# Kernel tuning notes

Hardware: AMD Instinct MI355X
Metric: run time of the kernel (lower is better)

The kernel has to match this reference:

```python
import jax, jax.numpy as jnp
import numpy as np

EPS = 1e-6  # torch nn.PairwiseDistance / TripletMarginLoss default eps (added elementwise to the difference)


def setup_inputs() -> dict:
    key = jax.random.key(0)
    k1, k2, k3, k4 = jax.random.split(key, 4)
    bs, d, n_classes = 4096, 2048, 64
    return {
        "h1": jax.random.normal(k1, (bs, d), dtype=jnp.float32),
        "h2": jax.random.normal(k2, (bs, d), dtype=jnp.float32),
        "labels1": jax.random.randint(k3, (bs,), 0, n_classes, dtype=jnp.int64),
        "labels2": jax.random.randint(k4, (bs,), 0, n_classes, dtype=jnp.int64),
    }


def _pairwise_dist_matrix(h1, h2):
    # torch PairwiseDistance: ||x - y + eps||_2. Expand the square to avoid
    # materializing the (bs, bs, d) broadcast tensor the torch code creates:
    d = h1.shape[-1]
    sq1 = jnp.sum(h1 * h1, axis=-1)          # (bs,)
    sq2 = jnp.sum(h2 * h2, axis=-1)          # (bs,)
    s1 = jnp.sum(h1, axis=-1)                # (bs,)
    s2 = jnp.sum(h2, axis=-1)                # (bs,)
    dot = jnp.einsum("id,jd->ij", h1, h2)   # (bs, bs) -- dominant GEMM
    dist2 = (sq1[:, None] + sq2[None, :] - 2.0 * dot
             + 2.0 * EPS * (s1[:, None] - s2[None, :]) + d * EPS * EPS)
    return jnp.sqrt(jnp.maximum(dist2, 0.0))


def reference(h1, h2, labels1, labels2):
    bs = h1.shape[0]
    h1 = h1.reshape(bs, -1)
    h2 = h2.reshape(bs, -1)

    dist_matrix = _pairwise_dist_matrix(h1, h2)              # (bs, bs)
    label_matrix = labels1[:, None] == labels2[None, :]       # (bs, bs) bool
    valid = jnp.any(label_matrix, axis=-1) & jnp.any(~label_matrix, axis=-1)

    # Hard positive: farthest same-label; hard negative: closest different-label.
    hard_pos_ids = jnp.argmax(jnp.where(label_matrix, dist_matrix, -jnp.inf), axis=-1)
    hard_neg_ids = jnp.argmin(jnp.where(label_matrix, jnp.inf, dist_matrix), axis=-1)

    pos = h2[hard_pos_ids]                                    # (bs, d) gather
    neg = h2[hard_neg_ids]                                    # (bs, d) gather

    d_ap = jnp.sqrt(jnp.sum(jnp.square(h1 - pos + EPS), axis=-1))
    d_an = jnp.sqrt(jnp.sum(jnp.square(h1 - neg + EPS), axis=-1))
    per_row = jnp.maximum(d_ap - d_an, 0.0)                   # margin = 0.0

    cnt = jnp.sum(valid.astype(jnp.float32))
    loss_sum = jnp.sum(jnp.where(valid, per_row, 0.0))
    # Matches torch: mean over valid triples, 0.0 if none are valid.
    return jnp.where(cnt > 0, loss_sum / jnp.maximum(cnt, 1.0), 0.0)
```

## Files before the change

kernel.cpp:

```cpp
#include <hip/hip_runtime.h>
#include <hip/hip_bf16.h>
#include <math.h>

#define BS 4096
#define DIM 2048
#define EPSV 1e-6f

typedef unsigned char u8;
typedef unsigned long long u64;
typedef long i64;
typedef float f32x4 __attribute__((ext_vector_type(4)));

__device__ inline u8 f2e4m3(float f) {
  unsigned u = __float_as_uint(f);
  unsigned s = (u >> 24) & 0x80u;
  unsigned ae = u & 0x7FFFFFFFu;
  if (ae < 0x3C800000u) return (u8)s;
  if (ae > 0x43E00000u) ae = 0x43E00000u;
  unsigned r = ae + 0x7FFFFu + ((ae >> 20) & 1u);
  unsigned e = (r >> 23) & 0xFFu;
  return (u8)(s | ((e - 120u) << 3) | ((r >> 20) & 7u));
}

__device__ inline void gload16(const u8* g, u8* l_) {
  __builtin_amdgcn_global_load_lds((const __attribute__((address_space(1))) unsigned int*)g,
                                   (__attribute__((address_space(3))) unsigned int*)l_,
                                   16, 0, 0);
}

__global__ __launch_bounds__(256) void prep_kernel(
    const float* __restrict__ h1, const float* __restrict__ h2,
    u8* __restrict__ A, u8* __restrict__ B,
    float* __restrict__ sq1, float* __restrict__ s1,
    float* __restrict__ sq2, float* __restrict__ s2) {
  int b = blockIdx.x;
  const float* src; u8* dst; float* sqo; float* so; int row;
  if (b < BS) { src = h1; dst = A; sqo = sq1; so = s1; row = b; }
  else        { src = h2; dst = B; sqo = sq2; so = s2; row = b - BS; }
  src += (size_t)row * DIM;
  dst += (size_t)row * DIM;
  int t = threadIdx.x;
  int idx = t * 8;
  float4 v0 = *(const float4*)(src + idx);
  float4 v1 = *(const float4*)(src + idx + 4);
  float sq = v0.x*v0.x + v0.y*v0.y + v0.z*v0.z + v0.w*v0.w
           + v1.x*v1.x + v1.y*v1.y + v1.z*v1.z + v1.w*v1.w;
  float s  = v0.x + v0.y + v0.z + v0.w + v1.x + v1.y + v1.z + v1.w;
  u64 pk = (u64)f2e4m3(v0.x)
         | ((u64)f2e4m3(v0.y) << 8)
         | ((u64)f2e4m3(v0.z) << 16)
         | ((u64)f2e4m3(v0.w) << 24)
         | ((u64)f2e4m3(v1.x) << 32)
         | ((u64)f2e4m3(v1.y) << 40)
         | ((u64)f2e4m3(v1.z) << 48)
         | ((u64)f2e4m3(v1.w) << 56);
  int vswz = (row >> 2) & 3;
  int dstIdx = (t >> 2) * 32 + (((t & 3) ^ vswz) << 3);
  *(u64*)(dst + dstIdx) = pk;
#pragma unroll
  for (int m = 32; m; m >>= 1) { sq += __shfl_xor(sq, m, 64); s += __shfl_xor(s, m, 64); }
  __shared__ float lsq[4], ls[4];
  if ((t & 63) == 0) { lsq[t >> 6] = sq; ls[t >> 6] = s; }
  __syncthreads();
  if (t == 0) {
    sqo[row] = lsq[0] + lsq[1] + lsq[2] + lsq[3];
    so[row]  = ls[0] + ls[1] + ls[2] + ls[3];
  }
}

#define BK 32
#define NT (DIM / BK)

__global__ __launch_bounds__(512, 4) void gemm_select_kernel(
    const u8* __restrict__ A, const u8* __restrict__ B,
    const float* __restrict__ sq1, const float* __restrict__ s1,
    const float* __restrict__ sq2, const float* __restrict__ s2,
    const int* __restrict__ lab1, const int* __restrict__ lab2,
    float4* __restrict__ part) {
  __shared__ __align__(16) u8 lds[2][12288];
  int tid = threadIdx.x;
  int w = tid >> 6, l = tid & 63;
  int wr = w >> 1, wc = w & 1;
  int g = l >> 4, c = l & 15;
  int by = blockIdx.x >> 5, bx = blockIdx.x & 31;
  const int rowB = by * 256, colB = bx * 128;

  int srow = tid >> 1;
  int khalf = (tid & 1) * 16;
  const u8* gA = A + (size_t)(rowB + srow) * DIM + khalf;
  const u8* gB = B + (size_t)(colB + (srow & 127)) * DIM + khalf;

#define STAGE(T) do { int b_ = (T) & 1; size_t k_ = (size_t)(T) * BK;  \
    gload16(gA + k_, &lds[b_][tid * 16]);                               \
    if (tid < 256) gload16(gB + k_, &lds[b_][8192 + tid * 16]); } while (0)

  const int slot = (g ^ ((c >> 2) & 3)) * 8;

  f32x4 acc[4][4] = {};

  STAGE(0);
  __syncthreads();

  for (int kt = 0; kt < NT; ++kt) {
    const u8* buf = lds[kt & 1];
    if (kt + 1 < NT) STAGE(kt + 1);
    i64 af[4], bfr[4];
#pragma unroll
    for (int mi = 0; mi < 4; ++mi)
      af[mi] = *(const i64*)&buf[(wr * 64 + mi * 16 + c) * 32 + slot];
#pragma unroll
    for (int ni = 0; ni < 4; ++ni)
      bfr[ni] = *(const i64*)&buf[8192 + (wc * 64 + ni * 16 + c) * 32 + slot];
#pragma unroll
    for (int mi = 0; mi < 4; ++mi)
#pragma unroll
      for (int ni = 0; ni < 4; ++ni)
        acc[mi][ni] = __builtin_amdgcn_mfma_f32_16x16x32_fp8_fp8(af[mi], bfr[ni], acc[mi][ni], 0, 0, 0);
    __syncthreads();
  }
#undef STAGE

  float pc_[4]; int l2v[4]; int jcol[4];
#pragma unroll
  for (int ni = 0; ni < 4; ++ni) {
    int j = colB + wc * 64 + ni * 16 + c;
    jcol[ni] = j;
    l2v[ni] = lab2[j];
    pc_[ni] = sq2[j] - 2.0f * EPSV * s2[j];
  }
  const float cst = (float)DIM * EPSV * EPSV;
  int partCol = bx * 2 + wc;

#pragma unroll
  for (int mi = 0; mi < 4; ++mi) {
    float posV[4], negV[4]; int posI[4], negI[4];
    float pr[4]; int l1v[4];
#pragma unroll
    for (int r = 0; r < 4; ++r) {
      int i = rowB + wr * 64 + mi * 16 + g * 4 + r;
      l1v[r] = lab1[i];
      pr[r] = sq1[i] + 2.0f * EPSV * s1[i] + cst;
      posV[r] = -3.0e38f; posI[r] = 0x7fffffff;
      negV[r] =  3.0e38f; negI[r] = 0x7fffffff;
    }
#pragma unroll
    for (int ni = 0; ni < 4; ++ni) {
#pragma unroll
      for (int r = 0; r < 4; ++r) {
        float dot = acc[mi][ni][r];
        float d2 = pr[r] + pc_[ni] - 2.0f * dot;
        float dist = sqrtf(fmaxf(d2, 0.0f));
        bool same = (l1v[r] == l2v[ni]);
        float pv = same ? dist : -3.0e38f;
        float nv = same ?  3.0e38f : dist;
        if (pv > posV[r] || (pv == posV[r] && jcol[ni] < posI[r])) { posV[r] = pv; posI[r] = jcol[ni]; }
        if (nv < negV[r] || (nv == negV[r] && jcol[ni] < negI[r])) { negV[r] = nv; negI[r] = jcol[ni]; }
      }
    }
#pragma unroll
    for (int m = 1; m < 16; m <<= 1) {
#pragma unroll
      for (int r = 0; r < 4; ++r) {
        float ov = __shfl_xor(posV[r], m, 64);
        int   oi = __shfl_xor(posI[r], m, 64);
        if (ov > posV[r] || (ov == posV[r] && oi < posI[r])) { posV[r] = ov; posI[r] = oi; }
        float nv2 = __shfl_xor(negV[r], m, 64);
        int   on  = __shfl_xor(negI[r], m, 64);
        if (nv2 < negV[r] || (nv2 == negV[r] && on < negI[r])) { negV[r] = nv2; negI[r] = on; }
      }
    }
    if (c == 0) {
#pragma unroll
      for (int r = 0; r < 4; ++r) {
        int i = rowB + wr * 64 + mi * 16 + g * 4 + r;
        float4 o;
        o.x = posV[r]; o.y = __int_as_float(posI[r]);
        o.z = negV[r]; o.w = __int_as_float(negI[r]);
        part[(size_t)i * 64 + partCol] = o;
      }
    }
  }
}

__global__ __launch_bounds__(256) void reduce_kernel(const float4* __restrict__ part,
                                                     float* __restrict__ perrow,
                                                     float* __restrict__ validf) {
  int row = blockIdx.x * 4 + (threadIdx.x >> 6);
  int lane = threadIdx.x & 63;
  float4 p = part[(size_t)row * 64 + lane];
  float posV = p.x; int posI = __float_as_int(p.y);
  float negV = p.z; int negI = __float_as_int(p.w);
#pragma unroll
  for (int m = 1; m < 64; m <<= 1) {
    float ov = __shfl_xor(posV, m, 64);
    int   oi = __shfl_xor(posI, m, 64);
    if (ov > posV || (ov == posV && oi < posI)) { posV = ov; posI = oi; }
    float nv = __shfl_xor(negV, m, 64);
    int   on = __shfl_xor(negI, m, 64);
    if (nv < negV || (nv == negV && on < negI)) { negV = nv; negI = on; }
  }
  if (lane == 0) {
    bool valid = (posV > -1.0e38f && negV < 1.0e38f);
    perrow[row] = valid ? fmaxf(posV - negV, 0.0f) : 0.0f;
    validf[row] = valid ? 1.0f : 0.0f;
  }
}

__global__ __launch_bounds__(256) void finalize_kernel(const float* __restrict__ perrow,
                                                       const float* __restrict__ validf,
                                                       float* __restrict__ out) {
  int t = threadIdx.x;
  float s = 0.f, cv = 0.f;
  for (int i = t; i < BS; i += 256) { s += perrow[i]; cv += validf[i]; }
  __shared__ float ls[256], lc[256];
  ls[t] = s; lc[t] = cv;
  __syncthreads();
  for (int m = 128; m; m >>= 1) {
    if (t < m) { ls[t] += ls[t + m]; lc[t] += lc[t + m]; }
    __syncthreads();
  }
  if (t == 0) out[0] = (lc[0] > 0.f) ? ls[0] / fmaxf(lc[0], 1.f) : 0.f;
}

extern "C" void kernel_launch(void* const* d_in, const int* in_sizes, int n_in,
                              void* d_out, int out_size, void* d_ws, size_t ws_size,
                              hipStream_t stream) {
  const float* h1 = (const float*)d_in[0];
  const float* h2 = (const float*)d_in[1];
  const int* lab1 = (const int*)d_in[2];
  const int* lab2 = (const int*)d_in[3];

  char* ws = (char*)d_ws;
  u8* A = (u8*)ws;
  u8* B = (u8*)(ws + (size_t)BS * DIM);
  size_t off = (size_t)BS * DIM * 2;
  float* sq1 = (float*)(ws + off); off += BS * 4;
  float* s1  = (float*)(ws + off); off += BS * 4;
  float* sq2 = (float*)(ws + off); off += BS * 4;
  float* s2  = (float*)(ws + off); off += BS * 4;
  float4* part = (float4*)(ws + off); off += (size_t)BS * 64 * 16;
  float* perrow = (float*)(ws + off); off += BS * 4;
  float* validf = (float*)(ws + off); off += BS * 4;

  prep_kernel<<<2 * BS, 256, 0, stream>>>(h1, h2, A, B, sq1, s1, sq2, s2);
  gemm_select_kernel<<<512, 512, 0, stream>>>(A, B, sq1, s1, sq2, s2, lab1, lab2, part);
  reduce_kernel<<<BS / 4, 256, 0, stream>>>(part, perrow, validf);
  finalize_kernel<<<1, 256, 0, stream>>>(perrow, validf, (float*)d_out);
}
```

Baseline: 101.4 us.

## Shrink FP8 GEMM block tile to 128x128 and deepen K staging to 128

Each block of the fused FP8 GEMM + hard-mining kernel now covers 128x128 outputs instead of 256x128, and the grid doubles to 1024 blocks. Each pipeline stage now loads a K chunk of 128 split into four 32-wide LDS sub-buffers, with A and B loads shared evenly across all threads. This cuts the number of barrier-separated iterations by four and gives more blocks to spread across CUs. In exchange, per-thread accumulators are halved, each B fragment gets less reuse, global reloads of B rise, and LDS per block grows to 64KB, which may limit how many blocks fit on a CU.

```diff
diff --git a/kernel.cpp b/kernel.cpp
--- a/kernel.cpp
+++ b/kernel.cpp
@@ -68,8 +68,8 @@
   }
 }
 
-#define BK 32
-#define NT (DIM / BK)
+#define BK128 128
+#define NT128 (DIM / BK128)
 
 __global__ __launch_bounds__(512, 4) void gemm_select_kernel(
     const u8* __restrict__ A, const u8* __restrict__ B,
@@ -77,45 +77,51 @@
     const float* __restrict__ sq2, const float* __restrict__ s2,
     const int* __restrict__ lab1, const int* __restrict__ lab2,
     float4* __restrict__ part) {
-  __shared__ __align__(16) u8 lds[2][12288];
+  __shared__ __align__(16) u8 lds[2][4][8192];
   int tid = threadIdx.x;
   int w = tid >> 6, l = tid & 63;
   int wr = w >> 1, wc = w & 1;
   int g = l >> 4, c = l & 15;
   int by = blockIdx.x >> 5, bx = blockIdx.x & 31;
-  const int rowB = by * 256, colB = bx * 128;
-
-  int srow = tid >> 1;
-  int khalf = (tid & 1) * 16;
-  const u8* gA = A + (size_t)(rowB + srow) * DIM + khalf;
-  const u8* gB = B + (size_t)(colB + (srow & 127)) * DIM + khalf;
-
-#define STAGE(T) do { int b_ = (T) & 1; size_t k_ = (size_t)(T) * BK;  \
-    gload16(gA + k_, &lds[b_][tid * 16]);                               \
-    if (tid < 256) gload16(gB + k_, &lds[b_][8192 + tid * 16]); } while (0)
+  const int rowB = by * 128, colB = bx * 128;
+
+  int t2 = tid & 255;
+  int srow = t2 >> 1;
+  int khalf = (t2 & 1) * 16;
+  const u8* gsrc = (tid < 256)
+      ? A + (size_t)(rowB + srow) * DIM + khalf
+      : B + (size_t)(colB + srow) * DIM + khalf;
+  int ldst = (tid < 256 ? 0 : 4096) + t2 * 16;
+
+#define STAGE(T) do { int b_ = (T) & 1; size_t k_ = (size_t)(T) * BK128;  \
+    _Pragma("unroll") for (int st_ = 0; st_ < 4; ++st_)                    \
+      gload16(gsrc + k_ + st_ * 32, &lds[b_][st_][ldst]); } while (0)
 
   const int slot = (g ^ ((c >> 2) & 3)) * 8;
 
-  f32x4 acc[4][4] = {};
+  f32x4 acc[2][4] = {};
 
   STAGE(0);
   __syncthreads();
 
-  for (int kt = 0; kt < NT; ++kt) {
-    const u8* buf = lds[kt & 1];
-    if (kt + 1 < NT) STAGE(kt + 1);
-    i64 af[4], bfr[4];
-#pragma unroll
-    for (int mi = 0; mi < 4; ++mi)
-      af[mi] = *(const i64*)&buf[(wr * 64 + mi * 16 + c) * 32 + slot];
-#pragma unroll
-    for (int ni = 0; ni < 4; ++ni)
-      bfr[ni] = *(const i64*)&buf[8192 + (wc * 64 + ni * 16 + c) * 32 + slot];
-#pragma unroll
-    for (int mi = 0; mi < 4; ++mi)
+  for (int kt = 0; kt < NT128; ++kt) {
+    if (kt + 1 < NT128) STAGE(kt + 1);
+#pragma unroll
+    for (int st = 0; st < 4; ++st) {
+      const u8* buf = lds[kt & 1][st];
+      i64 af[2], bfr[4];
+#pragma unroll
+      for (int mi = 0; mi < 2; ++mi)
+        af[mi] = *(const i64*)&buf[(wr * 32 + mi * 16 + c) * 32 + slot];
 #pragma unroll
       for (int ni = 0; ni < 4; ++ni)
-        acc[mi][ni] = __builtin_amdgcn_mfma_f32_16x16x32_fp8_fp8(af[mi], bfr[ni], acc[mi][ni], 0, 0, 0);
+        bfr[ni] = *(const i64*)&buf[4096 + (wc * 64 + ni * 16 + c) * 32 + slot];
+#pragma unroll
+      for (int mi = 0; mi < 2; ++mi)
+#pragma unroll
+        for (int ni = 0; ni < 4; ++ni)
+          acc[mi][ni] = __builtin_amdgcn_mfma_f32_16x16x32_fp8_fp8(af[mi], bfr[ni], acc[mi][ni], 0, 0, 0);
+    }
     __syncthreads();
   }
 #undef STAGE
@@ -132,12 +138,12 @@
   int partCol = bx * 2 + wc;
 
 #pragma unroll
-  for (int mi = 0; mi < 4; ++mi) {
+  for (int mi = 0; mi < 2; ++mi) {
     float posV[4], negV[4]; int posI[4], negI[4];
     float pr[4]; int l1v[4];
 #pragma unroll
     for (int r = 0; r < 4; ++r) {
-      int i = rowB + wr * 64 + mi * 16 + g * 4 + r;
+      int i = rowB + wr * 32 + mi * 16 + g * 4 + r;
       l1v[r] = lab1[i];
       pr[r] = sq1[i] + 2.0f * EPSV * s1[i] + cst;
       posV[r] = -3.0e38f; posI[r] = 0x7fffffff;
@@ -172,7 +178,7 @@
     if (c == 0) {
 #pragma unroll
       for (int r = 0; r < 4; ++r) {
-        int i = rowB + wr * 64 + mi * 16 + g * 4 + r;
+        int i = rowB + wr * 32 + mi * 16 + g * 4 + r;
         float4 o;
         o.x = posV[r]; o.y = __int_as_float(posI[r]);
         o.z = negV[r]; o.w = __int_as_float(negI[r]);
@@ -243,7 +249,7 @@
   float* validf = (float*)(ws + off); off += BS * 4;
 
   prep_kernel<<<2 * BS, 256, 0, stream>>>(h1, h2, A, B, sq1, s1, sq2, s2);
-  gemm_select_kernel<<<512, 512, 0, stream>>>(A, B, sq1, s1, sq2, s2, lab1, lab2, part);
+  gemm_select_kernel<<<1024, 512, 0, stream>>>(A, B, sq1, s1, sq2, s2, lab1, lab2, part);
   reduce_kernel<<<BS / 4, 256, 0, stream>>>(part, perrow, validf);
   finalize_kernel<<<1, 256, 0, stream>>>(perrow, validf, (float*)d_out);
 }
```

Measured after the change: 92.57 us. 8.7% less time.
